# Kernel tuning notes

Measured on AMD Instinct MI355X. Metric: run time of the kernel, lower is better.

## Reference

```python
import jax, jax.numpy as jnp
import numpy as np

N_NODES = 50000
N_EDGES = 600000
N_GRAPHS = 64
IN_DIM = 6
HID = 128


def setup_inputs() -> dict:
    key = jax.random.key(0)
    ks = jax.random.split(key, 10)
    x = jax.random.normal(ks[0], (N_NODES, IN_DIM), dtype=jnp.float32)
    edge_index = jax.random.randint(ks[1], (2, N_EDGES), 0, N_NODES, dtype=jnp.int64)
    batch = jnp.sort(jax.random.randint(ks[2], (N_NODES,), 0, N_GRAPHS, dtype=jnp.int64))
    def glorot(k, shape):
        lim = float(np.sqrt(6.0 / (shape[0] + shape[1])))
        return jax.random.uniform(k, shape, jnp.float32, -lim, lim)
    return {
        'x': x, 'edge_index': edge_index, 'batch': batch,
        'W1': glorot(ks[3], (IN_DIM, HID)), 'b1': jnp.zeros((HID,), jnp.float32),
        'W2': glorot(ks[4], (HID, HID)), 'b2': jnp.zeros((HID,), jnp.float32),
        'W3': glorot(ks[5], (HID, HID)), 'b3': jnp.zeros((HID,), jnp.float32),
        'fc1_w': glorot(ks[6], (HID, 64)), 'fc1_b': jnp.zeros((64,), jnp.float32),
        'fc2_w': glorot(ks[7], (64, 1)), 'fc2_b': jnp.zeros((1,), jnp.float32),
    }


def _gcn_norm(edge_index, n):
    # PyG GCNConv default: add self-loops, symmetric D^-1/2 A D^-1/2 normalization.
    loop = jnp.arange(n, dtype=edge_index.dtype)
    src = jnp.concatenate([edge_index[0], loop])
    dst = jnp.concatenate([edge_index[1], loop])
    deg = jax.ops.segment_sum(jnp.ones_like(dst, dtype=jnp.float32), dst, num_segments=n)
    dis = jnp.where(deg > 0, jax.lax.rsqrt(jnp.maximum(deg, 1.0)), 0.0)
    norm = dis[src] * dis[dst]  # [E+N]
    return src, dst, norm


def _gcn_layer(x, W, b, src, dst, norm, n):
    h = x @ W                       # [N, H] small GEMM
    msg = h[src] * norm[:, None]    # [E+N, H] irregular gather
    out = jax.ops.segment_sum(msg, dst, num_segments=n)  # scatter-add
    return out + b


def reference(x, edge_index, batch, W1, b1, W2, b2, W3, b3, fc1_w, fc1_b, fc2_w, fc2_b):
    n = x.shape[0]
    src, dst, norm = _gcn_norm(edge_index, n)
    h = jax.nn.relu(_gcn_layer(x, W1, b1, src, dst, norm, n))
    h = jax.nn.relu(_gcn_layer(h, W2, b2, src, dst, norm, n))
    h = jax.nn.relu(_gcn_layer(h, W3, b3, src, dst, norm, n))
    # global mean pool over graphs
    sums = jax.ops.segment_sum(h, batch, num_segments=N_GRAPHS)  # [B, H]
    cnt = jax.ops.segment_sum(jnp.ones((n,), jnp.float32), batch, num_segments=N_GRAPHS)
    pooled = sums / jnp.maximum(cnt, 1.0)[:, None]
    z = jax.nn.relu(pooled @ fc1_w + fc1_b)
    return z @ fc2_w + fc2_b  # [B, 1]
```

## Files before the change

### kernel.cpp

```cpp
#include <hip/hip_runtime.h>
#include <hip/hip_fp16.h>

#define HID 128
#define NGRAPH 64
#define CAP 64

typedef unsigned int uint32;
typedef unsigned short ushort;
using short8 = __attribute__((ext_vector_type(8))) short;
using f32x4  = __attribute__((ext_vector_type(4))) float;

__device__ __forceinline__ float2 h2f2(uint32 u) {
    __half2 h = *(__half2*)&u;
    return __half22float2(h);
}
__device__ __forceinline__ uint32 f2h2(float a, float b) {
    __half2 h;
    h.x = __float2half(a);
    h.y = __float2half(b);
    return *(uint32*)&h;
}

__global__ void setup(int* __restrict__ fill, uint32* __restrict__ s1,
                      uint32* __restrict__ s2, float* __restrict__ pooled,
                      int n, int npool) {
    int i = blockIdx.x * blockDim.x + threadIdx.x;
    if (i < n) fill[i] = 0;
    if (i < 64) {
        s1[(size_t)n * 64 + i] = 0u;
        s2[(size_t)n * 64 + i] = 0u;
    }
    if (i < npool) pooled[i] = 0.f;
}

__global__ void csr_fill_pack(const int* __restrict__ src, const int* __restrict__ dst,
                              int* __restrict__ fill, int* __restrict__ csr,
                              int E, int EB,
                              const float* __restrict__ W2, const float* __restrict__ W3,
                              ushort* __restrict__ wt) {
    int b = blockIdx.x;
    if (b < EB) {
        int e = b * blockDim.x + threadIdx.x;
        if (e >= E) return;
        int d = dst[e];
        int pos = atomicAdd(&fill[d], 1);
        if (pos < CAP) csr[(size_t)d * CAP + pos] = src[e];
    } else {
        int t = (b - EB) * blockDim.x + threadIdx.x;
        int sel = t >> 14;
        int idx = t & 16383;
        int nn = idx >> 7, kk = idx & 127;
        const float* W = sel ? W3 : W2;
        wt[sel * 16384 + idx] = __half_as_ushort(__float2half(W[kk * HID + nn]));
    }
}

__global__ void finalize(const int* __restrict__ fill, float* __restrict__ dis,
                         const float* __restrict__ x, float4* __restrict__ xp4, int n) {
    int i = blockIdx.x * blockDim.x + threadIdx.x;
    if (i >= n) return;
    int d = fill[i] + 1;
    float di = (float)(1.0 / sqrt((double)d));
    dis[i] = di;
    const float* xi = x + (size_t)i * 6;
    xp4[(size_t)i * 2]     = make_float4(di * xi[0], di * xi[1], di * xi[2], di * xi[3]);
    xp4[(size_t)i * 2 + 1] = make_float4(di * xi[4], di * xi[5], 0.f, 0.f);
}

__global__ __launch_bounds__(256) void layer1_fused(
    const float4* __restrict__ xp4, const int* __restrict__ fill,
    const int* __restrict__ csr, const float* __restrict__ dis,
    const float* __restrict__ W1, const float* __restrict__ b1,
    uint32* __restrict__ S1, int n) {
    int t = blockIdx.x * blockDim.x + threadIdx.x;
    int i = t >> 6, lane = t & 63;
    if (i >= n) return;
    int m = fill[i]; if (m > CAP) m = CAP;
    float a0 = 0.f, a1 = 0.f, a2 = 0.f, a3 = 0.f, a4 = 0.f, a5 = 0.f;
    if (lane < m) {
        int s = csr[(size_t)i * CAP + lane];
        float4 p0 = xp4[(size_t)s * 2];
        float4 p1 = xp4[(size_t)s * 2 + 1];
        a0 = p0.x; a1 = p0.y; a2 = p0.z;
        a3 = p0.w; a4 = p1.x; a5 = p1.y;
    }
#pragma unroll
    for (int off = 32; off > 0; off >>= 1) {
        a0 += __shfl_xor(a0, off); a1 += __shfl_xor(a1, off);
        a2 += __shfl_xor(a2, off); a3 += __shfl_xor(a3, off);
        a4 += __shfl_xor(a4, off); a5 += __shfl_xor(a5, off);
    }
    float di = dis[i];
    float4 s0 = xp4[(size_t)i * 2];
    float4 s1 = xp4[(size_t)i * 2 + 1];
    float xa[6];
    xa[0] = di * (s0.x + a0); xa[1] = di * (s0.y + a1);
    xa[2] = di * (s0.z + a2); xa[3] = di * (s0.w + a3);
    xa[4] = di * (s1.x + a4); xa[5] = di * (s1.y + a5);
    int c0 = lane * 2;
    float z0 = b1[c0], z1 = b1[c0 + 1];
#pragma unroll
    for (int k = 0; k < 6; ++k) {
        z0 += xa[k] * W1[k * HID + c0];
        z1 += xa[k] * W1[k * HID + c0 + 1];
    }
    S1[(size_t)i * 64 + lane] = f2h2(di * fmaxf(z0, 0.f), di * fmaxf(z1, 0.f));
}

__global__ __launch_bounds__(256) void layer_agg_gemm(
    const uint32* __restrict__ Sin, const int* __restrict__ fill,
    const int* __restrict__ csr, const float* __restrict__ dis,
    const ushort* __restrict__ WT, const float* __restrict__ bias,
    uint32* __restrict__ Sout, int n, int scaleOut) {
    __shared__ uint4 plds4[32 * 17];
    const int wave = threadIdx.x >> 6;
    const int lane = threadIdx.x & 63;
    const int grp = lane >> 4;
    const int q   = lane & 15;
    const int blk0 = blockIdx.x * 32;

    for (int j = 0; j < 8; ++j) {
        int row = wave * 8 + j;
        int i = blk0 + row;
        float acc[8] = {0.f, 0.f, 0.f, 0.f, 0.f, 0.f, 0.f, 0.f};
        if (i < n) {
            int m = fill[i]; if (m > CAP) m = CAP;
            int idx = (lane < m) ? csr[(size_t)i * CAP + lane] : n;
            uint4 sv = *(const uint4*)(Sin + (size_t)i * 64 + q * 4);
            float w0 = (grp == 0) ? 1.f : 0.f;
            { float2 d0 = h2f2(sv.x), d1 = h2f2(sv.y), d2 = h2f2(sv.z), d3 = h2f2(sv.w);
              acc[0] = w0 * d0.x; acc[1] = w0 * d0.y; acc[2] = w0 * d1.x; acc[3] = w0 * d1.y;
              acc[4] = w0 * d2.x; acc[5] = w0 * d2.y; acc[6] = w0 * d3.x; acc[7] = w0 * d3.y; }
            int remCeil = (m + 15) & ~15;
            for (int k = 0; k < remCeil; k += 16) {
                int s1 = __shfl(idx, k + grp);
                int s2 = __shfl(idx, k + 4 + grp);
                int s3 = __shfl(idx, k + 8 + grp);
                int s4 = __shfl(idx, k + 12 + grp);
                uint4 v1 = *(const uint4*)(Sin + (size_t)s1 * 64 + q * 4);
                uint4 v2 = *(const uint4*)(Sin + (size_t)s2 * 64 + q * 4);
                uint4 v3 = *(const uint4*)(Sin + (size_t)s3 * 64 + q * 4);
                uint4 v4 = *(const uint4*)(Sin + (size_t)s4 * 64 + q * 4);
                float2 e0, e1, e2, e3;
                e0 = h2f2(v1.x); e1 = h2f2(v1.y); e2 = h2f2(v1.z); e3 = h2f2(v1.w);
                acc[0] += e0.x; acc[1] += e0.y; acc[2] += e1.x; acc[3] += e1.y;
                acc[4] += e2.x; acc[5] += e2.y; acc[6] += e3.x; acc[7] += e3.y;
                e0 = h2f2(v2.x); e1 = h2f2(v2.y); e2 = h2f2(v2.z); e3 = h2f2(v2.w);
                acc[0] += e0.x; acc[1] += e0.y; acc[2] += e1.x; acc[3] += e1.y;
                acc[4] += e2.x; acc[5] += e2.y; acc[6] += e3.x; acc[7] += e3.y;
                e0 = h2f2(v3.x); e1 = h2f2(v3.y); e2 = h2f2(v3.z); e3 = h2f2(v3.w);
                acc[0] += e0.x; acc[1] += e0.y; acc[2] += e1.x; acc[3] += e1.y;
                acc[4] += e2.x; acc[5] += e2.y; acc[6] += e3.x; acc[7] += e3.y;
                e0 = h2f2(v4.x); e1 = h2f2(v4.y); e2 = h2f2(v4.z); e3 = h2f2(v4.w);
                acc[0] += e0.x; acc[1] += e0.y; acc[2] += e1.x; acc[3] += e1.y;
                acc[4] += e2.x; acc[5] += e2.y; acc[6] += e3.x; acc[7] += e3.y;
            }
#pragma unroll
            for (int r = 0; r < 8; ++r) {
                acc[r] += __shfl_xor(acc[r], 16);
                acc[r] += __shfl_xor(acc[r], 32);
            }
        }
        if (grp == 0) {
            float d = (i < n) ? dis[i] : 0.f;
            uint4 h4 = make_uint4(f2h2(d * acc[0], d * acc[1]),
                                  f2h2(d * acc[2], d * acc[3]),
                                  f2h2(d * acc[4], d * acc[5]),
                                  f2h2(d * acc[6], d * acc[7]));
            plds4[row * 17 + q] = h4;
        }
    }
    __syncthreads();

    const int l16 = lane & 15, quad = lane >> 4;
    f32x4 acc2[2][2] = {};
#pragma unroll
    for (int kc = 0; kc < 4; ++kc) {
        int ko = kc * 32 + quad * 8;
        short8 a0 = *(const short8*)&plds4[(size_t)l16 * 17 + kc * 4 + quad];
        short8 a1 = *(const short8*)&plds4[(size_t)(16 + l16) * 17 + kc * 4 + quad];
#pragma unroll
        for (int ct = 0; ct < 2; ++ct) {
            short8 wh = *(const short8*)(WT + (size_t)(wave * 32 + ct * 16 + l16) * HID + ko);
            acc2[0][ct] = __builtin_amdgcn_mfma_f32_16x16x32_f16(wh, a0, acc2[0][ct], 0, 0, 0);
            acc2[1][ct] = __builtin_amdgcn_mfma_f32_16x16x32_f16(wh, a1, acc2[1][ct], 0, 0, 0);
        }
    }
    ushort* so = (ushort*)Sout;
#pragma unroll
    for (int rt = 0; rt < 2; ++rt) {
        int node = blk0 + rt * 16 + l16;
        if (node >= n) continue;
        float sc = scaleOut ? dis[node] : 1.f;
#pragma unroll
        for (int ct = 0; ct < 2; ++ct) {
            int cb = wave * 32 + ct * 16 + quad * 4;
            float4 bv = *(const float4*)(bias + cb);
            float o0 = fmaxf(acc2[rt][ct][0] + bv.x, 0.f) * sc;
            float o1 = fmaxf(acc2[rt][ct][1] + bv.y, 0.f) * sc;
            float o2 = fmaxf(acc2[rt][ct][2] + bv.z, 0.f) * sc;
            float o3 = fmaxf(acc2[rt][ct][3] + bv.w, 0.f) * sc;
            *(uint2*)(so + (size_t)node * HID + cb) = make_uint2(f2h2(o0, o1), f2h2(o2, o3));
        }
    }
}

#define POOL_CHUNK 64
__global__ void pool_partial(const uint32* __restrict__ h, const int* __restrict__ batch,
                             float* __restrict__ pooled, int* __restrict__ gcnt, int n) {
    int c = threadIdx.x;
    int start = blockIdx.x * POOL_CHUNK;
    if (start >= n) return;
    int end = start + POOL_CHUNK;
    if (end > n) end = n;
    int curg = batch[start];
    float sx = 0.f, sy = 0.f;
    int cnt = 0;
    for (int i = start; i < end; ++i) {
        int g = batch[i];
        if (g != curg) {
            atomicAdd(&pooled[curg * HID + 2 * c], sx);
            atomicAdd(&pooled[curg * HID + 2 * c + 1], sy);
            if (c == 0) atomicAdd(&gcnt[curg], cnt);
            sx = 0.f; sy = 0.f; cnt = 0;
            curg = g;
        }
        float2 v = h2f2(h[(size_t)i * 64 + c]);
        sx += v.x; sy += v.y;
        ++cnt;
    }
    atomicAdd(&pooled[curg * HID + 2 * c], sx);
    atomicAdd(&pooled[curg * HID + 2 * c + 1], sy);
    if (c == 0) atomicAdd(&gcnt[curg], cnt);
}

__global__ void mlp_head(const float* __restrict__ pooled, const int* __restrict__ cnt,
                         const float* __restrict__ fc1w, const float* __restrict__ fc1b,
                         const float* __restrict__ fc2w, const float* __restrict__ fc2b,
                         float* __restrict__ out) {
    int g = blockIdx.x;
    int j = threadIdx.x;
    float inv = 1.0f / fmaxf((float)cnt[g], 1.0f);
    float z = fc1b[j];
    for (int k = 0; k < HID; ++k) z += (pooled[g * HID + k] * inv) * fc1w[k * 64 + j];
    z = fmaxf(z, 0.f);
    float v = z * fc2w[j];
#pragma unroll
    for (int off = 32; off > 0; off >>= 1) v += __shfl_down(v, off);
    if (j == 0) out[g] = v + fc2b[0];
}

extern "C" void kernel_launch(void* const* d_in, const int* in_sizes, int n_in,
                              void* d_out, int out_size, void* d_ws, size_t ws_size,
                              hipStream_t stream) {
    const float* x     = (const float*)d_in[0];
    const int*   ei    = (const int*)d_in[1];
    const int*   batch = (const int*)d_in[2];
    const float* W1    = (const float*)d_in[3];
    const float* b1    = (const float*)d_in[4];
    const float* W2    = (const float*)d_in[5];
    const float* b2    = (const float*)d_in[6];
    const float* W3    = (const float*)d_in[7];
    const float* b3    = (const float*)d_in[8];
    const float* fc1w  = (const float*)d_in[9];
    const float* fc1b  = (const float*)d_in[10];
    const float* fc2w  = (const float*)d_in[11];
    const float* fc2b  = (const float*)d_in[12];
    float* out = (float*)d_out;

    const int N = in_sizes[0] / 6;
    const int E = in_sizes[1] / 2;
    const int* src = ei;
    const int* dst = ei + E;

    char* ws = (char*)d_ws;
    char* p = ws;
    uint32* S1   = (uint32*)p;   p += (size_t)(N + 1) * 256;
    uint32* S2   = (uint32*)p;   p += (size_t)(N + 1) * 256;
    uint32* B1h  = (uint32*)p;   p += (size_t)N * 256;
    float4* xp4  = (float4*)p;   p += (size_t)N * 32;
    ushort* WT   = (ushort*)p;   p += 2 * 32768;
    float* dis     = (float*)p;  p += (size_t)N * 4;
    int*   fill    = (int*)p;    p += (size_t)N * 4;
    int*   csr     = (int*)p;    p += (size_t)N * CAP * 4;
    float* pooled  = (float*)p;  p += (size_t)NGRAPH * HID * 4;
    int*   gcnt    = (int*)p;

    const int B = 256;
    const int EB = (E + B - 1) / B;
    const int npool = NGRAPH * HID + NGRAPH;

    setup<<<(N + B - 1) / B, B, 0, stream>>>(fill, S1, S2, pooled, N, npool);
    csr_fill_pack<<<EB + 128, B, 0, stream>>>(src, dst, fill, csr, E, EB, W2, W3, WT);
    finalize<<<(N + B - 1) / B, B, 0, stream>>>(fill, dis, x, xp4, N);

    int nodeWaveBlocks = (int)(((size_t)N * 64 + B - 1) / B);
    int fusedBlocks = (N + 31) / 32;

    layer1_fused<<<nodeWaveBlocks, B, 0, stream>>>(xp4, fill, csr, dis, W1, b1, S1, N);

    layer_agg_gemm<<<fusedBlocks, B, 0, stream>>>(S1, fill, csr, dis, WT, b2, S2, N, 1);

    layer_agg_gemm<<<fusedBlocks, B, 0, stream>>>(S2, fill, csr, dis, WT + 16384, b3, B1h, N, 0);

    pool_partial<<<(N + POOL_CHUNK - 1) / POOL_CHUNK, 64, 0, stream>>>(B1h, batch, pooled, gcnt, N);

    mlp_head<<<NGRAPH, 64, 0, stream>>>(pooled, gcnt, fc1w, fc1b, fc2w, fc2b, out);
}
```

Before: 247.0 us.

## Interleave two rows' neighbor gathers and fold self-loop into CSR index list

The aggregation loop now preloads the CSR indices for all 8 rows a wave handles, then processes rows in pairs. It issues eight independent gathers up front for the first 16 neighbors of both rows, which raises memory-level parallelism and hides gather latency. The self-loop term is put into the index list at slot m instead of being loaded separately. Launch bounds now ask for 5 blocks per CU, which limits registers and risks spills given the larger live state (idx8, two accumulators).

Result: faster. 234.9 us (-4.9%).

```diff
diff --git a/kernel.cpp b/kernel.cpp
--- a/kernel.cpp
+++ b/kernel.cpp
@@ -19,6 +19,12 @@
     h.x = __float2half(a);
     h.y = __float2half(b);
     return *(uint32*)&h;
+}
+
+__device__ __forceinline__ void accum4(float* acc, uint4 v) {
+    float2 e0 = h2f2(v.x), e1 = h2f2(v.y), e2 = h2f2(v.z), e3 = h2f2(v.w);
+    acc[0] += e0.x; acc[1] += e0.y; acc[2] += e1.x; acc[3] += e1.y;
+    acc[4] += e2.x; acc[5] += e2.y; acc[6] += e3.x; acc[7] += e3.y;
 }
 
 __global__ void setup(int* __restrict__ fill, uint32* __restrict__ s1,
@@ -107,7 +113,7 @@
     S1[(size_t)i * 64 + lane] = f2h2(di * fmaxf(z0, 0.f), di * fmaxf(z1, 0.f));
 }
 
-__global__ __launch_bounds__(256) void layer_agg_gemm(
+__global__ __launch_bounds__(256, 5) void layer_agg_gemm(
     const uint32* __restrict__ Sin, const int* __restrict__ fill,
     const int* __restrict__ csr, const float* __restrict__ dis,
     const ushort* __restrict__ WT, const float* __restrict__ bias,
@@ -118,56 +124,92 @@
     const int grp = lane >> 4;
     const int q   = lane & 15;
     const int blk0 = blockIdx.x * 32;
-
+    const int base = blk0 + wave * 8;
+
+    int mt8[8];
+    int idx8[8];
+#pragma unroll
     for (int j = 0; j < 8; ++j) {
-        int row = wave * 8 + j;
-        int i = blk0 + row;
-        float acc[8] = {0.f, 0.f, 0.f, 0.f, 0.f, 0.f, 0.f, 0.f};
-        if (i < n) {
-            int m = fill[i]; if (m > CAP) m = CAP;
-            int idx = (lane < m) ? csr[(size_t)i * CAP + lane] : n;
-            uint4 sv = *(const uint4*)(Sin + (size_t)i * 64 + q * 4);
-            float w0 = (grp == 0) ? 1.f : 0.f;
-            { float2 d0 = h2f2(sv.x), d1 = h2f2(sv.y), d2 = h2f2(sv.z), d3 = h2f2(sv.w);
-              acc[0] = w0 * d0.x; acc[1] = w0 * d0.y; acc[2] = w0 * d1.x; acc[3] = w0 * d1.y;
-              acc[4] = w0 * d2.x; acc[5] = w0 * d2.y; acc[6] = w0 * d3.x; acc[7] = w0 * d3.y; }
-            int remCeil = (m + 15) & ~15;
-            for (int k = 0; k < remCeil; k += 16) {
-                int s1 = __shfl(idx, k + grp);
-                int s2 = __shfl(idx, k + 4 + grp);
-                int s3 = __shfl(idx, k + 8 + grp);
-                int s4 = __shfl(idx, k + 12 + grp);
-                uint4 v1 = *(const uint4*)(Sin + (size_t)s1 * 64 + q * 4);
-                uint4 v2 = *(const uint4*)(Sin + (size_t)s2 * 64 + q * 4);
-                uint4 v3 = *(const uint4*)(Sin + (size_t)s3 * 64 + q * 4);
-                uint4 v4 = *(const uint4*)(Sin + (size_t)s4 * 64 + q * 4);
-                float2 e0, e1, e2, e3;
-                e0 = h2f2(v1.x); e1 = h2f2(v1.y); e2 = h2f2(v1.z); e3 = h2f2(v1.w);
-                acc[0] += e0.x; acc[1] += e0.y; acc[2] += e1.x; acc[3] += e1.y;
-                acc[4] += e2.x; acc[5] += e2.y; acc[6] += e3.x; acc[7] += e3.y;
-                e0 = h2f2(v2.x); e1 = h2f2(v2.y); e2 = h2f2(v2.z); e3 = h2f2(v2.w);
-                acc[0] += e0.x; acc[1] += e0.y; acc[2] += e1.x; acc[3] += e1.y;
-                acc[4] += e2.x; acc[5] += e2.y; acc[6] += e3.x; acc[7] += e3.y;
-                e0 = h2f2(v3.x); e1 = h2f2(v3.y); e2 = h2f2(v3.z); e3 = h2f2(v3.w);
-                acc[0] += e0.x; acc[1] += e0.y; acc[2] += e1.x; acc[3] += e1.y;
-                acc[4] += e2.x; acc[5] += e2.y; acc[6] += e3.x; acc[7] += e3.y;
-                e0 = h2f2(v4.x); e1 = h2f2(v4.y); e2 = h2f2(v4.z); e3 = h2f2(v4.w);
-                acc[0] += e0.x; acc[1] += e0.y; acc[2] += e1.x; acc[3] += e1.y;
-                acc[4] += e2.x; acc[5] += e2.y; acc[6] += e3.x; acc[7] += e3.y;
-            }
-#pragma unroll
-            for (int r = 0; r < 8; ++r) {
-                acc[r] += __shfl_xor(acc[r], 16);
-                acc[r] += __shfl_xor(acc[r], 32);
-            }
+        int i = base + j;
+        int fv = (i < n) ? fill[i] : 0;
+        int m = fv > CAP ? CAP : fv;
+        idx8[j] = (lane < m) ? csr[(size_t)i * CAP + lane]
+                             : ((lane == m && i < n && m < CAP) ? i : n);
+        mt8[j] = m + (m < CAP ? 1 : 0);
+    }
+
+#pragma unroll
+    for (int jp = 0; jp < 4; ++jp) {
+        const int ja = jp * 2, jb = ja + 1;
+        float acca[8] = {0.f, 0.f, 0.f, 0.f, 0.f, 0.f, 0.f, 0.f};
+        float accb[8] = {0.f, 0.f, 0.f, 0.f, 0.f, 0.f, 0.f, 0.f};
+        {
+            int sa1 = __shfl(idx8[ja], grp);
+            int sa2 = __shfl(idx8[ja], 4 + grp);
+            int sa3 = __shfl(idx8[ja], 8 + grp);
+            int sa4 = __shfl(idx8[ja], 12 + grp);
+            int sb1 = __shfl(idx8[jb], grp);
+            int sb2 = __shfl(idx8[jb], 4 + grp);
+            int sb3 = __shfl(idx8[jb], 8 + grp);
+            int sb4 = __shfl(idx8[jb], 12 + grp);
+            uint4 va1 = *(const uint4*)(Sin + (size_t)sa1 * 64 + q * 4);
+            uint4 va2 = *(const uint4*)(Sin + (size_t)sa2 * 64 + q * 4);
+            uint4 va3 = *(const uint4*)(Sin + (size_t)sa3 * 64 + q * 4);
+            uint4 va4 = *(const uint4*)(Sin + (size_t)sa4 * 64 + q * 4);
+            uint4 vb1 = *(const uint4*)(Sin + (size_t)sb1 * 64 + q * 4);
+            uint4 vb2 = *(const uint4*)(Sin + (size_t)sb2 * 64 + q * 4);
+            uint4 vb3 = *(const uint4*)(Sin + (size_t)sb3 * 64 + q * 4);
+            uint4 vb4 = *(const uint4*)(Sin + (size_t)sb4 * 64 + q * 4);
+            accum4(acca, va1); accum4(acca, va2);
+            accum4(acca, va3); accum4(acca, va4);
+            accum4(accb, vb1); accum4(accb, vb2);
+            accum4(accb, vb3); accum4(accb, vb4);
+        }
+        for (int k = 16; k < mt8[ja]; k += 16) {
+            int s1 = __shfl(idx8[ja], k + grp);
+            int s2 = __shfl(idx8[ja], k + 4 + grp);
+            int s3 = __shfl(idx8[ja], k + 8 + grp);
+            int s4 = __shfl(idx8[ja], k + 12 + grp);
+            uint4 v1 = *(const uint4*)(Sin + (size_t)s1 * 64 + q * 4);
+            uint4 v2 = *(const uint4*)(Sin + (size_t)s2 * 64 + q * 4);
+            uint4 v3 = *(const uint4*)(Sin + (size_t)s3 * 64 + q * 4);
+            uint4 v4 = *(const uint4*)(Sin + (size_t)s4 * 64 + q * 4);
+            accum4(acca, v1); accum4(acca, v2);
+            accum4(acca, v3); accum4(acca, v4);
+        }
+        for (int k = 16; k < mt8[jb]; k += 16) {
+            int s1 = __shfl(idx8[jb], k + grp);
+            int s2 = __shfl(idx8[jb], k + 4 + grp);
+            int s3 = __shfl(idx8[jb], k + 8 + grp);
+            int s4 = __shfl(idx8[jb], k + 12 + grp);
+            uint4 v1 = *(const uint4*)(Sin + (size_t)s1 * 64 + q * 4);
+            uint4 v2 = *(const uint4*)(Sin + (size_t)s2 * 64 + q * 4);
+            uint4 v3 = *(const uint4*)(Sin + (size_t)s3 * 64 + q * 4);
+            uint4 v4 = *(const uint4*)(Sin + (size_t)s4 * 64 + q * 4);
+            accum4(accb, v1); accum4(accb, v2);
+            accum4(accb, v3); accum4(accb, v4);
+        }
+#pragma unroll
+        for (int r = 0; r < 8; ++r) {
+            acca[r] += __shfl_xor(acca[r], 16);
+            acca[r] += __shfl_xor(acca[r], 32);
+            accb[r] += __shfl_xor(accb[r], 16);
+            accb[r] += __shfl_xor(accb[r], 32);
         }
         if (grp == 0) {
-            float d = (i < n) ? dis[i] : 0.f;
-            uint4 h4 = make_uint4(f2h2(d * acc[0], d * acc[1]),
-                                  f2h2(d * acc[2], d * acc[3]),
-                                  f2h2(d * acc[4], d * acc[5]),
-                                  f2h2(d * acc[6], d * acc[7]));
-            plds4[row * 17 + q] = h4;
+            int ia = base + ja, ib = base + jb;
+            float da = (ia < n) ? dis[ia] : 0.f;
+            float db = (ib < n) ? dis[ib] : 0.f;
+            plds4[(wave * 8 + ja) * 17 + q] =
+                make_uint4(f2h2(da * acca[0], da * acca[1]),
+                           f2h2(da * acca[2], da * acca[3]),
+                           f2h2(da * acca[4], da * acca[5]),
+                           f2h2(da * acca[6], da * acca[7]));
+            plds4[(wave * 8 + jb) * 17 + q] =
+                make_uint4(f2h2(db * accb[0], db * accb[1]),
+                           f2h2(db * accb[2], db * accb[3]),
+                           f2h2(db * accb[4], db * accb[5]),
+                           f2h2(db * accb[6], db * accb[7]));
         }
     }
     __syncthreads();
```

## Batch gathers across nodes in aggregation; fuse pooling with MLP head

Applied to the files above, without the earlier changes.

The aggregation+GEMM kernel now handles 16 nodes per block instead of 32, which doubles the grid. Each wave issues the first-chunk neighbor gathers for its 4 nodes up front, so more loads are in flight. The self-loop term is folded into the neighbor index list, and launch bounds are set for higher occupancy. Pooling and the MLP head are merged into one kernel per graph that binary-searches the sorted batch array, which removes the atomics, the pooled-buffer zeroing and one launch, at the cost of only 64 blocks doing the pooling reads.

Result: no change. 243.5 us (-1.4%).

```diff
diff --git a/kernel.cpp b/kernel.cpp
--- a/kernel.cpp
+++ b/kernel.cpp
@@ -4,6 +4,7 @@
 #define HID 128
 #define NGRAPH 64
 #define CAP 64
+#define NPB 16
 
 typedef unsigned int uint32;
 typedef unsigned short ushort;
@@ -21,16 +22,32 @@
     return *(uint32*)&h;
 }
 
+__device__ __forceinline__ void accum4(float* acc, uint4 v) {
+    float2 e0 = h2f2(v.x), e1 = h2f2(v.y), e2 = h2f2(v.z), e3 = h2f2(v.w);
+    acc[0] += e0.x; acc[1] += e0.y; acc[2] += e1.x; acc[3] += e1.y;
+    acc[4] += e2.x; acc[5] += e2.y; acc[6] += e3.x; acc[7] += e3.y;
+}
+
+__device__ __forceinline__ void issue4(const uint32* __restrict__ Sin, int idxv,
+                                       int grp, int q, uint4* r) {
+    int s1 = __shfl(idxv, grp);
+    int s2 = __shfl(idxv, 4 + grp);
+    int s3 = __shfl(idxv, 8 + grp);
+    int s4 = __shfl(idxv, 12 + grp);
+    r[0] = *(const uint4*)(Sin + (size_t)s1 * 64 + q * 4);
+    r[1] = *(const uint4*)(Sin + (size_t)s2 * 64 + q * 4);
+    r[2] = *(const uint4*)(Sin + (size_t)s3 * 64 + q * 4);
+    r[3] = *(const uint4*)(Sin + (size_t)s4 * 64 + q * 4);
+}
+
 __global__ void setup(int* __restrict__ fill, uint32* __restrict__ s1,
-                      uint32* __restrict__ s2, float* __restrict__ pooled,
-                      int n, int npool) {
+                      uint32* __restrict__ s2, int n) {
     int i = blockIdx.x * blockDim.x + threadIdx.x;
     if (i < n) fill[i] = 0;
     if (i < 64) {
         s1[(size_t)n * 64 + i] = 0u;
         s2[(size_t)n * 64 + i] = 0u;
     }
-    if (i < npool) pooled[i] = 0.f;
 }
 
 __global__ void csr_fill_pack(const int* __restrict__ src, const int* __restrict__ dst,
@@ -107,147 +124,208 @@
     S1[(size_t)i * 64 + lane] = f2h2(di * fmaxf(z0, 0.f), di * fmaxf(z1, 0.f));
 }
 
-__global__ __launch_bounds__(256) void layer_agg_gemm(
+__global__ __launch_bounds__(256, 4) void layer_agg_gemm(
     const uint32* __restrict__ Sin, const int* __restrict__ fill,
     const int* __restrict__ csr, const float* __restrict__ dis,
     const ushort* __restrict__ WT, const float* __restrict__ bias,
     uint32* __restrict__ Sout, int n, int scaleOut) {
-    __shared__ uint4 plds4[32 * 17];
+    __shared__ uint4 plds4[NPB * 17];
     const int wave = threadIdx.x >> 6;
     const int lane = threadIdx.x & 63;
     const int grp = lane >> 4;
     const int q   = lane & 15;
-    const int blk0 = blockIdx.x * 32;
-
-    for (int j = 0; j < 8; ++j) {
-        int row = wave * 8 + j;
-        int i = blk0 + row;
-        float acc[8] = {0.f, 0.f, 0.f, 0.f, 0.f, 0.f, 0.f, 0.f};
-        if (i < n) {
-            int m = fill[i]; if (m > CAP) m = CAP;
-            int idx = (lane < m) ? csr[(size_t)i * CAP + lane] : n;
-            uint4 sv = *(const uint4*)(Sin + (size_t)i * 64 + q * 4);
-            float w0 = (grp == 0) ? 1.f : 0.f;
-            { float2 d0 = h2f2(sv.x), d1 = h2f2(sv.y), d2 = h2f2(sv.z), d3 = h2f2(sv.w);
-              acc[0] = w0 * d0.x; acc[1] = w0 * d0.y; acc[2] = w0 * d1.x; acc[3] = w0 * d1.y;
-              acc[4] = w0 * d2.x; acc[5] = w0 * d2.y; acc[6] = w0 * d3.x; acc[7] = w0 * d3.y; }
-            int remCeil = (m + 15) & ~15;
-            for (int k = 0; k < remCeil; k += 16) {
-                int s1 = __shfl(idx, k + grp);
-                int s2 = __shfl(idx, k + 4 + grp);
-                int s3 = __shfl(idx, k + 8 + grp);
-                int s4 = __shfl(idx, k + 12 + grp);
-                uint4 v1 = *(const uint4*)(Sin + (size_t)s1 * 64 + q * 4);
-                uint4 v2 = *(const uint4*)(Sin + (size_t)s2 * 64 + q * 4);
-                uint4 v3 = *(const uint4*)(Sin + (size_t)s3 * 64 + q * 4);
-                uint4 v4 = *(const uint4*)(Sin + (size_t)s4 * 64 + q * 4);
-                float2 e0, e1, e2, e3;
-                e0 = h2f2(v1.x); e1 = h2f2(v1.y); e2 = h2f2(v1.z); e3 = h2f2(v1.w);
-                acc[0] += e0.x; acc[1] += e0.y; acc[2] += e1.x; acc[3] += e1.y;
-                acc[4] += e2.x; acc[5] += e2.y; acc[6] += e3.x; acc[7] += e3.y;
-                e0 = h2f2(v2.x); e1 = h2f2(v2.y); e2 = h2f2(v2.z); e3 = h2f2(v2.w);
-                acc[0] += e0.x; acc[1] += e0.y; acc[2] += e1.x; acc[3] += e1.y;
-                acc[4] += e2.x; acc[5] += e2.y; acc[6] += e3.x; acc[7] += e3.y;
-                e0 = h2f2(v3.x); e1 = h2f2(v3.y); e2 = h2f2(v3.z); e3 = h2f2(v3.w);
-                acc[0] += e0.x; acc[1] += e0.y; acc[2] += e1.x; acc[3] += e1.y;
-                acc[4] += e2.x; acc[5] += e2.y; acc[6] += e3.x; acc[7] += e3.y;
-                e0 = h2f2(v4.x); e1 = h2f2(v4.y); e2 = h2f2(v4.z); e3 = h2f2(v4.w);
-                acc[0] += e0.x; acc[1] += e0.y; acc[2] += e1.x; acc[3] += e1.y;
-                acc[4] += e2.x; acc[5] += e2.y; acc[6] += e3.x; acc[7] += e3.y;
-            }
-#pragma unroll
-            for (int r = 0; r < 8; ++r) {
-                acc[r] += __shfl_xor(acc[r], 16);
-                acc[r] += __shfl_xor(acc[r], 32);
-            }
-        }
-        if (grp == 0) {
-            float d = (i < n) ? dis[i] : 0.f;
-            uint4 h4 = make_uint4(f2h2(d * acc[0], d * acc[1]),
-                                  f2h2(d * acc[2], d * acc[3]),
-                                  f2h2(d * acc[4], d * acc[5]),
-                                  f2h2(d * acc[6], d * acc[7]));
-            plds4[row * 17 + q] = h4;
-        }
+    const int blk0 = blockIdx.x * NPB;
+    const int base = blk0 + wave * 4;
+
+    int mt4[4];
+    int idx4[4];
+#pragma unroll
+    for (int j = 0; j < 4; ++j) {
+        int i = base + j;
+        int fv = (i < n) ? fill[i] : 0;
+        int m = fv > CAP ? CAP : fv;
+        idx4[j] = (lane < m) ? csr[(size_t)i * CAP + lane]
+                             : ((lane == m && i < n && m < CAP) ? i : n);
+        mt4[j] = (i < n) ? (m + (m < CAP ? 1 : 0)) : 0;
+    }
+
+    uint4 va[4], vb[4], wa[4], wb[4];
+    issue4(Sin, idx4[0], grp, q, va);
+    issue4(Sin, idx4[1], grp, q, vb);
+    issue4(Sin, idx4[2], grp, q, wa);
+    issue4(Sin, idx4[3], grp, q, wb);
+
+    float acc0[8], acc1[8];
+#pragma unroll
+    for (int r = 0; r < 8; ++r) { acc0[r] = 0.f; acc1[r] = 0.f; }
+    accum4(acc0, va[0]); accum4(acc0, va[1]); accum4(acc0, va[2]); accum4(acc0, va[3]);
+    accum4(acc1, vb[0]); accum4(acc1, vb[1]); accum4(acc1, vb[2]); accum4(acc1, vb[3]);
+    for (int k = 16; k < mt4[0]; k += 16) {
+        uint4 r4[4];
+        int s1 = __shfl(idx4[0], k + grp), s2 = __shfl(idx4[0], k + 4 + grp);
+        int s3 = __shfl(idx4[0], k + 8 + grp), s4 = __shfl(idx4[0], k + 12 + grp);
+        r4[0] = *(const uint4*)(Sin + (size_t)s1 * 64 + q * 4);
+        r4[1] = *(const uint4*)(Sin + (size_t)s2 * 64 + q * 4);
+        r4[2] = *(const uint4*)(Sin + (size_t)s3 * 64 + q * 4);
+        r4[3] = *(const uint4*)(Sin + (size_t)s4 * 64 + q * 4);
+        accum4(acc0, r4[0]); accum4(acc0, r4[1]); accum4(acc0, r4[2]); accum4(acc0, r4[3]);
+    }
+    for (int k = 16; k < mt4[1]; k += 16) {
+        uint4 r4[4];
+        int s1 = __shfl(idx4[1], k + grp), s2 = __shfl(idx4[1], k + 4 + grp);
+        int s3 = __shfl(idx4[1], k + 8 + grp), s4 = __shfl(idx4[1], k + 12 + grp);
+        r4[0] = *(const uint4*)(Sin + (size_t)s1 * 64 + q * 4);
+        r4[1] = *(const uint4*)(Sin + (size_t)s2 * 64 + q * 4);
+        r4[2] = *(const uint4*)(Sin + (size_t)s3 * 64 + q * 4);
+        r4[3] = *(const uint4*)(Sin + (size_t)s4 * 64 + q * 4);
+        accum4(acc1, r4[0]); accum4(acc1, r4[1]); accum4(acc1, r4[2]); accum4(acc1, r4[3]);
+    }
+#pragma unroll
+    for (int r = 0; r < 8; ++r) {
+        acc0[r] += __shfl_xor(acc0[r], 16); acc0[r] += __shfl_xor(acc0[r], 32);
+        acc1[r] += __shfl_xor(acc1[r], 16); acc1[r] += __shfl_xor(acc1[r], 32);
+    }
+    if (grp == 0) {
+        int ia = base, ib = base + 1;
+        float da = (ia < n) ? dis[ia] : 0.f;
+        float db = (ib < n) ? dis[ib] : 0.f;
+        plds4[(wave * 4 + 0) * 17 + q] =
+            make_uint4(f2h2(da * acc0[0], da * acc0[1]), f2h2(da * acc0[2], da * acc0[3]),
+                       f2h2(da * acc0[4], da * acc0[5]), f2h2(da * acc0[6], da * acc0[7]));
+        plds4[(wave * 4 + 1) * 17 + q] =
+            make_uint4(f2h2(db * acc1[0], db * acc1[1]), f2h2(db * acc1[2], db * acc1[3]),
+                       f2h2(db * acc1[4], db * acc1[5]), f2h2(db * acc1[6], db * acc1[7]));
+    }
+#pragma unroll
+    for (int r = 0; r < 8; ++r) { acc0[r] = 0.f; acc1[r] = 0.f; }
+    accum4(acc0, wa[0]); accum4(acc0, wa[1]); accum4(acc0, wa[2]); accum4(acc0, wa[3]);
+    accum4(acc1, wb[0]); accum4(acc1, wb[1]); accum4(acc1, wb[2]); accum4(acc1, wb[3]);
+    for (int k = 16; k < mt4[2]; k += 16) {
+        uint4 r4[4];
+        int s1 = __shfl(idx4[2], k + grp), s2 = __shfl(idx4[2], k + 4 + grp);
+        int s3 = __shfl(idx4[2], k + 8 + grp), s4 = __shfl(idx4[2], k + 12 + grp);
+        r4[0] = *(const uint4*)(Sin + (size_t)s1 * 64 + q * 4);
+        r4[1] = *(const uint4*)(Sin + (size_t)s2 * 64 + q * 4);
+        r4[2] = *(const uint4*)(Sin + (size_t)s3 * 64 + q * 4);
+        r4[3] = *(const uint4*)(Sin + (size_t)s4 * 64 + q * 4);
+        accum4(acc0, r4[0]); accum4(acc0, r4[1]); accum4(acc0, r4[2]); accum4(acc0, r4[3]);
+    }
+    for (int k = 16; k < mt4[3]; k += 16) {
+        uint4 r4[4];
+        int s1 = __shfl(idx4[3], k + grp), s2 = __shfl(idx4[3], k + 4 + grp);
+        int s3 = __shfl(idx4[3], k + 8 + grp), s4 = __shfl(idx4[3], k + 12 + grp);
+        r4[0] = *(const uint4*)(Sin + (size_t)s1 * 64 + q * 4);
+        r4[1] = *(const uint4*)(Sin + (size_t)s2 * 64 + q * 4);
+        r4[2] = *(const uint4*)(Sin + (size_t)s3 * 64 + q * 4);
+        r4[3] = *(const uint4*)(Sin + (size_t)s4 * 64 + q * 4);
+        accum4(acc1, r4[0]); accum4(acc1, r4[1]); accum4(acc1, r4[2]); accum4(acc1, r4[3]);
+    }
+#pragma unroll
+    for (int r = 0; r < 8; ++r) {
+        acc0[r] += __shfl_xor(acc0[r], 16); acc0[r] += __shfl_xor(acc0[r], 32);
+        acc1[r] += __shfl_xor(acc1[r], 16); acc1[r] += __shfl_xor(acc1[r], 32);
+    }
+    if (grp == 0) {
+        int ia = base + 2, ib = base + 3;
+        float da = (ia < n) ? dis[ia] : 0.f;
+        float db = (ib < n) ? dis[ib] : 0.f;
+        plds4[(wave * 4 + 2) * 17 + q] =
+            make_uint4(f2h2(da * acc0[0], da * acc0[1]), f2h2(da * acc0[2], da * acc0[3]),
+                       f2h2(da * acc0[4], da * acc0[5]), f2h2(da * acc0[6], da * acc0[7]));
+        plds4[(wave * 4 + 3) * 17 + q] =
+            make_uint4(f2h2(db * acc1[0], db * acc1[1]), f2h2(db * acc1[2], db * acc1[3]),
+                       f2h2(db * acc1[4], db * acc1[5]), f2h2(db * acc1[6], db * acc1[7]));
     }
     __syncthreads();
 
     const int l16 = lane & 15, quad = lane >> 4;
-    f32x4 acc2[2][2] = {};
+    f32x4 acc2[2] = {};
 #pragma unroll
     for (int kc = 0; kc < 4; ++kc) {
         int ko = kc * 32 + quad * 8;
         short8 a0 = *(const short8*)&plds4[(size_t)l16 * 17 + kc * 4 + quad];
-        short8 a1 = *(const short8*)&plds4[(size_t)(16 + l16) * 17 + kc * 4 + quad];
 #pragma unroll
         for (int ct = 0; ct < 2; ++ct) {
             short8 wh = *(const short8*)(WT + (size_t)(wave * 32 + ct * 16 + l16) * HID + ko);
-            acc2[0][ct] = __builtin_amdgcn_mfma_f32_16x16x32_f16(wh, a0, acc2[0][ct], 0, 0, 0);
-            acc2[1][ct] = __builtin_amdgcn_mfma_f32_16x16x32_f16(wh, a1, acc2[1][ct], 0, 0, 0);
+            acc2[ct] = __builtin_amdgcn_mfma_f32_16x16x32_f16(wh, a0, acc2[ct], 0, 0, 0);
         }
     }
     ushort* so = (ushort*)Sout;
-#pragma unroll
-    for (int rt = 0; rt < 2; ++rt) {
-        int node = blk0 + rt * 16 + l16;
-        if (node >= n) continue;
+    int node = blk0 + l16;
+    if (node < n) {
         float sc = scaleOut ? dis[node] : 1.f;
 #pragma unroll
         for (int ct = 0; ct < 2; ++ct) {
             int cb = wave * 32 + ct * 16 + quad * 4;
             float4 bv = *(const float4*)(bias + cb);
-            float o0 = fmaxf(acc2[rt][ct][0] + bv.x, 0.f) * sc;
-            float o1 = fmaxf(acc2[rt][ct][1] + bv.y, 0.f) * sc;
-            float o2 = fmaxf(acc2[rt][ct][2] + bv.z, 0.f) * sc;
-            float o3 = fmaxf(acc2[rt][ct][3] + bv.w, 0.f) * sc;
+            float o0 = fmaxf(acc2[ct][0] + bv.x, 0.f) * sc;
+            float o1 = fmaxf(acc2[ct][1] + bv.y, 0.f) * sc;
+            float o2 = fmaxf(acc2[ct][2] + bv.z, 0.f) * sc;
+            float o3 = fmaxf(acc2[ct][3] + bv.w, 0.f) * sc;
             *(uint2*)(so + (size_t)node * HID + cb) = make_uint2(f2h2(o0, o1), f2h2(o2, o3));
         }
     }
 }
 
-#define POOL_CHUNK 64
-__global__ void pool_partial(const uint32* __restrict__ h, const int* __restrict__ batch,
-                             float* __restrict__ pooled, int* __restrict__ gcnt, int n) {
-    int c = threadIdx.x;
-    int start = blockIdx.x * POOL_CHUNK;
-    if (start >= n) return;
-    int end = start + POOL_CHUNK;
-    if (end > n) end = n;
-    int curg = batch[start];
+__global__ __launch_bounds__(256) void pool_head(
+    const uint32* __restrict__ h, const int* __restrict__ batch,
+    const float* __restrict__ fc1w, const float* __restrict__ fc1b,
+    const float* __restrict__ fc2w, const float* __restrict__ fc2b,
+    float* __restrict__ out, int n) {
+    __shared__ float red[4][128];
+    __shared__ float pp[128];
+    const int g = blockIdx.x;
+    const int t = threadIdx.x;
+    const int sub = t >> 6, c = t & 63;
+
+    int lo0 = 0, hi0 = n, lo1 = 0, hi1 = n;
+    while (lo0 < hi0 || lo1 < hi1) {
+        if (lo0 < hi0) {
+            int mid = (lo0 + hi0) >> 1;
+            if (batch[mid] < g) lo0 = mid + 1; else hi0 = mid;
+        }
+        if (lo1 < hi1) {
+            int mid = (lo1 + hi1) >> 1;
+            if (batch[mid] < g + 1) lo1 = mid + 1; else hi1 = mid;
+        }
+    }
+    const int start = lo0, end = lo1;
+
     float sx = 0.f, sy = 0.f;
-    int cnt = 0;
-    for (int i = start; i < end; ++i) {
-        int g = batch[i];
-        if (g != curg) {
-            atomicAdd(&pooled[curg * HID + 2 * c], sx);
-            atomicAdd(&pooled[curg * HID + 2 * c + 1], sy);
-            if (c == 0) atomicAdd(&gcnt[curg], cnt);
-            sx = 0.f; sy = 0.f; cnt = 0;
-            curg = g;
-        }
+    int i = start + sub;
+    for (; i + 12 < end; i += 16) {
+        uint32 u0 = h[(size_t)i * 64 + c];
+        uint32 u1 = h[(size_t)(i + 4) * 64 + c];
+        uint32 u2 = h[(size_t)(i + 8) * 64 + c];
+        uint32 u3 = h[(size_t)(i + 12) * 64 + c];
+        float2 v0 = h2f2(u0), v1 = h2f2(u1), v2 = h2f2(u2), v3 = h2f2(u3);
+        sx += v0.x + v1.x + v2.x + v3.x;
+        sy += v0.y + v1.y + v2.y + v3.y;
+    }
+    for (; i < end; i += 4) {
         float2 v = h2f2(h[(size_t)i * 64 + c]);
         sx += v.x; sy += v.y;
-        ++cnt;
-    }
-    atomicAdd(&pooled[curg * HID + 2 * c], sx);
-    atomicAdd(&pooled[curg * HID + 2 * c + 1], sy);
-    if (c == 0) atomicAdd(&gcnt[curg], cnt);
-}
-
-__global__ void mlp_head(const float* __restrict__ pooled, const int* __restrict__ cnt,
-                         const float* __restrict__ fc1w, const float* __restrict__ fc1b,
-                         const float* __restrict__ fc2w, const float* __restrict__ fc2b,
-                         float* __restrict__ out) {
-    int g = blockIdx.x;
-    int j = threadIdx.x;
-    float inv = 1.0f / fmaxf((float)cnt[g], 1.0f);
-    float z = fc1b[j];
-    for (int k = 0; k < HID; ++k) z += (pooled[g * HID + k] * inv) * fc1w[k * 64 + j];
-    z = fmaxf(z, 0.f);
-    float v = z * fc2w[j];
-#pragma unroll
-    for (int off = 32; off > 0; off >>= 1) v += __shfl_down(v, off);
-    if (j == 0) out[g] = v + fc2b[0];
+    }
+    *(float2*)&red[sub][2 * c] = make_float2(sx, sy);
+    __syncthreads();
+
+    if (t < 64) {
+        float2 r0 = *(float2*)&red[0][2 * t];
+        float2 r1 = *(float2*)&red[1][2 * t];
+        float2 r2 = *(float2*)&red[2][2 * t];
+        float2 r3 = *(float2*)&red[3][2 * t];
+        float inv = 1.0f / fmaxf((float)(end - start), 1.0f);
+        pp[2 * t]     = (r0.x + r1.x + r2.x + r3.x) * inv;
+        pp[2 * t + 1] = (r0.y + r1.y + r2.y + r3.y) * inv;
+        float z = fc1b[t];
+#pragma unroll 8
+        for (int k = 0; k < HID; ++k) z += pp[k] * fc1w[k * 64 + t];
+        z = fmaxf(z, 0.f);
+        float v = z * fc2w[t];
+#pragma unroll
+        for (int off = 32; off > 0; off >>= 1) v += __shfl_down(v, off);
+        if (t == 0) out[g] = v + fc2b[0];
+    }
 }
 
 extern "C" void kernel_launch(void* const* d_in, const int* in_sizes, int n_in,
@@ -283,19 +361,16 @@
     float* dis     = (float*)p;  p += (size_t)N * 4;
     int*   fill    = (int*)p;    p += (size_t)N * 4;
     int*   csr     = (int*)p;    p += (size_t)N * CAP * 4;
-    float* pooled  = (float*)p;  p += (size_t)NGRAPH * HID * 4;
-    int*   gcnt    = (int*)p;
 
     const int B = 256;
     const int EB = (E + B - 1) / B;
-    const int npool = NGRAPH * HID + NGRAPH;
-
-    setup<<<(N + B - 1) / B, B, 0, stream>>>(fill, S1, S2, pooled, N, npool);
+
+    setup<<<(N + B - 1) / B, B, 0, stream>>>(fill, S1, S2, N);
     csr_fill_pack<<<EB + 128, B, 0, stream>>>(src, dst, fill, csr, E, EB, W2, W3, WT);
     finalize<<<(N + B - 1) / B, B, 0, stream>>>(fill, dis, x, xp4, N);
 
     int nodeWaveBlocks = (int)(((size_t)N * 64 + B - 1) / B);
-    int fusedBlocks = (N + 31) / 32;
+    int fusedBlocks = (N + NPB - 1) / NPB;
 
     layer1_fused<<<nodeWaveBlocks, B, 0, stream>>>(xp4, fill, csr, dis, W1, b1, S1, N);
 
@@ -303,7 +378,5 @@
 
     layer_agg_gemm<<<fusedBlocks, B, 0, stream>>>(S2, fill, csr, dis, WT + 16384, b3, B1h, N, 0);
 
-    pool_partial<<<(N + POOL_CHUNK - 1) / POOL_CHUNK, 64, 0, stream>>>(B1h, batch, pooled, gcnt, N);
-
-    mlp_head<<<NGRAPH, 64, 0, stream>>>(pooled, gcnt, fc1w, fc1b, fc2w, fc2b, out);
-}
+    pool_head<<<NGRAPH, B, 0, stream>>>(B1h, batch, fc1w, fc1b, fc2w, fc2b, out, N);
+}
```
